# Kernel tuning notes

Hardware: AMD Instinct MI355X
Metric: run time of the kernel (lower is better)

## Reference

```python
import jax, jax.numpy as jnp
import numpy as np

N_NODES = 50000
N_EDGES = 600000
D_IN = 128
D_HID = 128
D_OUT = 128
LN_EPS = 1e-5


def _layer_norm(h, g, b):
    mu = jnp.mean(h, axis=-1, keepdims=True)
    var = jnp.var(h, axis=-1, keepdims=True)
    return (h - mu) * jax.lax.rsqrt(var + LN_EPS) * g + b


def _gin_conv(x, src, dst, w1, b1, w2, b2):
    # sum-aggregate neighbor messages at destination nodes, eps = 0
    agg = jax.ops.segment_sum(x[src], dst, num_segments=x.shape[0])
    h = x + agg
    h = jax.nn.relu(h @ w1 + b1)
    return h @ w2 + b2


def setup_inputs() -> dict:
    key = jax.random.key(0)
    ks = jax.random.split(key, 20)
    x = jax.random.normal(ks[0], (N_NODES, D_IN), dtype=jnp.float32)
    edge_index = jax.random.randint(ks[1], (2, N_EDGES), 0, N_NODES, dtype=jnp.int64)
    dims = [(D_IN, D_HID), (D_HID, D_HID), (D_HID, D_HID), (D_HID, D_OUT)]
    inp = {"x": x, "edge_index": edge_index}
    for i, (din, dout) in enumerate(dims):
        s1 = 1.0 / np.sqrt(din)
        s2 = 1.0 / np.sqrt(D_HID)
        inp[f"w1_{i}"] = jax.random.uniform(ks[2 + 4 * i], (din, D_HID), jnp.float32, -s1, s1)
        inp[f"b1_{i}"] = jax.random.uniform(ks[3 + 4 * i], (D_HID,), jnp.float32, -s1, s1)
        inp[f"w2_{i}"] = jax.random.uniform(ks[4 + 4 * i], (D_HID, dout), jnp.float32, -s2, s2)
        inp[f"b2_{i}"] = jax.random.uniform(ks[5 + 4 * i], (dout,), jnp.float32, -s2, s2)
    for i in range(3):  # LayerNorm only on first 3 blocks
        inp[f"g_{i}"] = jnp.ones((D_HID,), jnp.float32)
        inp[f"beta_{i}"] = jnp.zeros((D_HID,), jnp.float32)
    return inp


def reference(x, edge_index,
              w1_0, b1_0, w2_0, b2_0,
              w1_1, b1_1, w2_1, b2_1,
              w1_2, b1_2, w2_2, b2_2,
              w1_3, b1_3, w2_3, b2_3,
              g_0, beta_0, g_1, beta_1, g_2, beta_2):
    src, dst = edge_index[0], edge_index[1]
    mlps = [(w1_0, b1_0, w2_0, b2_0), (w1_1, b1_1, w2_1, b2_1),
            (w1_2, b1_2, w2_2, b2_2), (w1_3, b1_3, w2_3, b2_3)]
    lns = [(g_0, beta_0), (g_1, beta_1), (g_2, beta_2)]
    h = x
    for i in range(3):
        h = _gin_conv(h, src, dst, *mlps[i])
        h = _layer_norm(h, *lns[i])
        h = jax.nn.relu(h)  # dropout rate 0.0 -> identity
    h = _gin_conv(h, src, dst, *mlps[3])  # final block: no norm/act
    return h
```

## Files before the change

### kernel.cpp

```cpp
#include <hip/hip_runtime.h>
#include <hip/hip_bf16.h>

#define NN 50000
#define NE 600000
#define DD 128
#define LDSW 136
#define NB 196
#define BSH 8
#define EPB 2048
#define NBLK_AC ((NE + EPB - 1) / EPB)

typedef __bf16 bf16;
typedef __attribute__((ext_vector_type(8))) __bf16 bf16x8;
typedef __attribute__((ext_vector_type(4))) float f32x4;
typedef __attribute__((ext_vector_type(4))) unsigned int u32x4;
typedef __attribute__((ext_vector_type(4))) unsigned short u16x4;
typedef unsigned short u16;

__device__ __forceinline__ float bf_lo(unsigned int u) {
    return __builtin_bit_cast(float, u << 16);
}
__device__ __forceinline__ float bf_hi(unsigned int u) {
    return __builtin_bit_cast(float, u & 0xffff0000u);
}
__device__ __forceinline__ unsigned int bf_pack(float x, float y) {
    u16 a = __builtin_bit_cast(u16, (bf16)x);
    u16 b = __builtin_bit_cast(u16, (bf16)y);
    return (unsigned int)a | ((unsigned int)b << 16);
}

struct Ptr8 { const float* p[8]; };

__device__ __forceinline__ int edge_dst(const int* ei, int e, int f) {
    return f ? ei[2 * NE + 2 * e] : ei[NE + e];
}
__device__ __forceinline__ int edge_src(const int* ei, int e, int f) {
    return f ? ei[2 * e] : ei[e];
}

#define J1 (NN * DD / 4)
#define J2 (J1 + 8 * DD * DD)

__global__ __launch_bounds__(256) void k_init(const float* __restrict__ x,
                                              u16* __restrict__ xb,
                                              Ptr8 ws, u16* __restrict__ wt,
                                              int* __restrict__ bcnt,
                                              const int* __restrict__ ei,
                                              int* __restrict__ flag) {
    int tid = threadIdx.x;
    if (blockIdx.x == 0) {
        if (tid == 0) flag[0] = 1;
        __syncthreads();
        if (ei[2 * tid + 1] != 0) flag[0] = 0;
    }
    int id = blockIdx.x * 256 + tid;
    if (id < NB) bcnt[id] = 0;
    if (id < J1) {
        f32x4 v = *(const f32x4*)(x + (size_t)id * 4);
        u16x4 o;
        o.x = __builtin_bit_cast(u16, (bf16)v.x);
        o.y = __builtin_bit_cast(u16, (bf16)v.y);
        o.z = __builtin_bit_cast(u16, (bf16)v.z);
        o.w = __builtin_bit_cast(u16, (bf16)v.w);
        *(u16x4*)(xb + (size_t)id * 4) = o;
    } else if (id < J2) {
        int i = id - J1;
        int m = i >> 14;
        int rem = i & 16383;
        int k = rem >> 7;
        int n = rem & 127;
        bf16 b = (bf16)ws.p[m][k * DD + n];
        wt[(size_t)m * DD * DD + n * DD + k] = __builtin_bit_cast(u16, b);
    }
}

__global__ __launch_bounds__(256) void k_bcount(const int* __restrict__ ei,
                                                const int* __restrict__ flag,
                                                int* __restrict__ bcnt) {
    __shared__ int lh[NB];
    int tid = threadIdx.x;
    if (tid < NB) lh[tid] = 0;
    __syncthreads();
    int f = flag[0];
#pragma unroll
    for (int k = 0; k < 8; k++) {
        int e = blockIdx.x * EPB + k * 256 + tid;
        if (e < NE) {
            int d = edge_dst(ei, e, f);
            atomicAdd(&lh[d >> BSH], 1);
        }
    }
    __syncthreads();
    if (tid < NB && lh[tid] > 0) atomicAdd(&bcnt[tid], lh[tid]);
}

__global__ __launch_bounds__(256) void k_bscan(const int* __restrict__ bcnt,
                                               int* __restrict__ boff,
                                               int* __restrict__ bcur) {
    int tid = threadIdx.x;
    int lane = tid & 63, w = tid >> 6;
    int v = (tid < NB) ? bcnt[tid] : 0;
    int orig = v;
#pragma unroll
    for (int off = 1; off < 64; off <<= 1) {
        int t = __shfl_up(v, off);
        if (lane >= off) v += t;
    }
    __shared__ int sm[4];
    if (lane == 63) sm[w] = v;
    __syncthreads();
    int add = 0;
    for (int k = 0; k < w; k++) add += sm[k];
    int ex = v - orig + add;
    if (tid < NB) { boff[tid] = ex; bcur[tid] = ex; }
    if (tid == 0) boff[NB] = NE;
}

__global__ __launch_bounds__(256) void k_bscatter(const int* __restrict__ ei,
                                                  const int* __restrict__ flag,
                                                  int* __restrict__ bcur,
                                                  unsigned int* __restrict__ tmp) {
    __shared__ int lh[NB];
    __shared__ int gb[NB];
    int tid = threadIdx.x;
    if (tid < NB) lh[tid] = 0;
    __syncthreads();
    int f = flag[0];
    int src[8], dst[8], lp[8];
    bool val[8];
#pragma unroll
    for (int k = 0; k < 8; k++) {
        int e = blockIdx.x * EPB + k * 256 + tid;
        val[k] = (e < NE);
        if (val[k]) {
            src[k] = edge_src(ei, e, f);
            dst[k] = edge_dst(ei, e, f);
            lp[k] = atomicAdd(&lh[dst[k] >> BSH], 1);
        }
    }
    __syncthreads();
    if (tid < NB && lh[tid] > 0) gb[tid] = atomicAdd(&bcur[tid], lh[tid]);
    __syncthreads();
#pragma unroll
    for (int k = 0; k < 8; k++) {
        if (val[k]) {
            unsigned int pk = (unsigned)src[k] | ((unsigned)(dst[k] & 255) << 16);
            tmp[gb[dst[k] >> BSH] + lp[k]] = pk;
        }
    }
}

__global__ __launch_bounds__(256) void k_build(const unsigned int* __restrict__ tmp,
                                               const int* __restrict__ boff,
                                               int* __restrict__ row_start,
                                               int* __restrict__ adj) {
    __shared__ int cnt[256];
    __shared__ int ccur[256];
    __shared__ int sm[4];
    int b = blockIdx.x, tid = threadIdx.x;
    int base = b << BSH;
    int s = boff[b], e = boff[b + 1];
    cnt[tid] = 0;
    __syncthreads();
    for (int i = s + tid; i < e; i += 256) {
        atomicAdd(&cnt[tmp[i] >> 16], 1);
    }
    __syncthreads();
    int v = cnt[tid];
    int orig = v;
    int lane = tid & 63, w = tid >> 6;
#pragma unroll
    for (int off = 1; off < 64; off <<= 1) {
        int t = __shfl_up(v, off);
        if (lane >= off) v += t;
    }
    if (lane == 63) sm[w] = v;
    __syncthreads();
    int add = 0;
    for (int k = 0; k < w; k++) add += sm[k];
    int ex = s + (v - orig) + add;
    ccur[tid] = ex;
    if (base + tid < NN) row_start[base + tid] = ex;
    if (b == 0 && tid == 0) row_start[NN] = NE;
    __syncthreads();
    for (int i = s + tid; i < e; i += 256) {
        unsigned int pk = tmp[i];
        int p = atomicAdd(&ccur[pk >> 16], 1);
        adj[p] = (int)(pk & 0xffffu);
    }
}

__global__ __launch_bounds__(256) void k_agg(const u16* __restrict__ xb,
                                             const int* __restrict__ row_start,
                                             const int* __restrict__ adj,
                                             u16* __restrict__ out) {
    int gid = blockIdx.x * blockDim.x + threadIdx.x;
    int wave = gid >> 6, lane = gid & 63;
    int grp = lane >> 4, l = lane & 15;
    int node = wave * 4 + grp;
    if (node >= NN) return;
    const u32x4* base = (const u32x4*)xb;
    u32x4 sv = base[(size_t)node * 16 + l];
    float af[8], bf[8];
#pragma unroll
    for (int j = 0; j < 4; j++) {
        af[2 * j] = bf_lo(sv[j]); af[2 * j + 1] = bf_hi(sv[j]);
        bf[2 * j] = 0.f; bf[2 * j + 1] = 0.f;
    }
    int s = row_start[node], e = row_start[node + 1];
    int i = s;
    for (; i + 3 < e; i += 4) {
        u32x4 t0 = base[(size_t)adj[i] * 16 + l];
        u32x4 t1 = base[(size_t)adj[i + 1] * 16 + l];
        u32x4 t2 = base[(size_t)adj[i + 2] * 16 + l];
        u32x4 t3 = base[(size_t)adj[i + 3] * 16 + l];
#pragma unroll
        for (int j = 0; j < 4; j++) {
            af[2 * j]     += bf_lo(t0[j]) + bf_lo(t1[j]);
            af[2 * j + 1] += bf_hi(t0[j]) + bf_hi(t1[j]);
            bf[2 * j]     += bf_lo(t2[j]) + bf_lo(t3[j]);
            bf[2 * j + 1] += bf_hi(t2[j]) + bf_hi(t3[j]);
        }
    }
    for (; i < e; i++) {
        u32x4 t = base[(size_t)adj[i] * 16 + l];
#pragma unroll
        for (int j = 0; j < 4; j++) { af[2 * j] += bf_lo(t[j]); af[2 * j + 1] += bf_hi(t[j]); }
    }
    u32x4 o;
#pragma unroll
    for (int j = 0; j < 4; j++) o[j] = bf_pack(af[2 * j] + bf[2 * j], af[2 * j + 1] + bf[2 * j + 1]);
    ((u32x4*)out)[(size_t)node * 16 + l] = o;
}

template <bool LN, bool B16OUT>
__global__ __launch_bounds__(128) void k_mlp(const u16* __restrict__ hin,
                                             const u16* __restrict__ w1t,
                                             const float* __restrict__ b1,
                                             const u16* __restrict__ w2t,
                                             const float* __restrict__ b2,
                                             const float* __restrict__ g,
                                             const float* __restrict__ bta,
                                             void* __restrict__ hout) {
    __shared__ u16 lds[64 * LDSW];
    const int tid = threadIdx.x;
    const int wv = tid >> 6, lane = tid & 63;
    const int l15 = lane & 15, l4 = lane >> 4;
    const int tile0 = blockIdx.x * 64;

#pragma unroll
    for (int it = 0; it < 8; ++it) {
        int slot = tid + it * 128;
        int row = slot >> 4, c16 = slot & 15;
        u32x4 v = {0u, 0u, 0u, 0u};
        int grow = tile0 + row;
        if (grow < NN) v = *(const u32x4*)(hin + (size_t)grow * DD + c16 * 8);
        *(u32x4*)&lds[row * LDSW + c16 * 8] = v;
    }
    __syncthreads();

    float b1c[8], b2c[8], gc[8], bc[8];
#pragma unroll
    for (int c = 0; c < 8; c++) {
        int col = c * 16 + l15;
        b1c[c] = b1[col];
        b2c[c] = b2[col];
        if (LN) { gc[c] = g[col]; bc[c] = bta[col]; }
    }

    f32x4 acc[2][8];
#pragma unroll
    for (int r = 0; r < 2; r++)
#pragma unroll
        for (int c = 0; c < 8; c++) acc[r][c] = (f32x4){0.f, 0.f, 0.f, 0.f};

    const int rowbase = wv * 32;

#pragma unroll
    for (int ks = 0; ks < 4; ++ks) {
        bf16x8 a0 = __builtin_bit_cast(bf16x8,
            *(const u32x4*)&lds[(rowbase + l15) * LDSW + ks * 32 + l4 * 8]);
        bf16x8 a1 = __builtin_bit_cast(bf16x8,
            *(const u32x4*)&lds[(rowbase + 16 + l15) * LDSW + ks * 32 + l4 * 8]);
#pragma unroll
        for (int c = 0; c < 8; c++) {
            bf16x8 b = __builtin_bit_cast(bf16x8,
                *(const u32x4*)(w1t + (size_t)(c * 16 + l15) * DD + ks * 32 + l4 * 8));
            acc[0][c] = __builtin_amdgcn_mfma_f32_16x16x32_bf16(a0, b, acc[0][c], 0, 0, 0);
            acc[1][c] = __builtin_amdgcn_mfma_f32_16x16x32_bf16(a1, b, acc[1][c], 0, 0, 0);
        }
    }

#pragma unroll
    for (int r = 0; r < 2; r++) {
#pragma unroll
        for (int c = 0; c < 8; c++) {
            int col = c * 16 + l15;
#pragma unroll
            for (int j = 0; j < 4; j++) {
                float v = acc[r][c][j] + b1c[c];
                v = v > 0.f ? v : 0.f;
                bf16 b = (bf16)v;
                int row = rowbase + r * 16 + l4 * 4 + j;
                lds[row * LDSW + col] = __builtin_bit_cast(u16, b);
            }
        }
    }

#pragma unroll
    for (int r = 0; r < 2; r++)
#pragma unroll
        for (int c = 0; c < 8; c++) acc[r][c] = (f32x4){0.f, 0.f, 0.f, 0.f};

#pragma unroll
    for (int ks = 0; ks < 4; ++ks) {
        bf16x8 a0 = __builtin_bit_cast(bf16x8,
            *(const u32x4*)&lds[(rowbase + l15) * LDSW + ks * 32 + l4 * 8]);
        bf16x8 a1 = __builtin_bit_cast(bf16x8,
            *(const u32x4*)&lds[(rowbase + 16 + l15) * LDSW + ks * 32 + l4 * 8]);
#pragma unroll
        for (int c = 0; c < 8; c++) {
            bf16x8 b = __builtin_bit_cast(bf16x8,
                *(const u32x4*)(w2t + (size_t)(c * 16 + l15) * DD + ks * 32 + l4 * 8));
            acc[0][c] = __builtin_amdgcn_mfma_f32_16x16x32_bf16(a0, b, acc[0][c], 0, 0, 0);
            acc[1][c] = __builtin_amdgcn_mfma_f32_16x16x32_bf16(a1, b, acc[1][c], 0, 0, 0);
        }
    }

#pragma unroll
    for (int r = 0; r < 2; r++) {
        float vals[8][4];
#pragma unroll
        for (int c = 0; c < 8; c++)
#pragma unroll
            for (int j = 0; j < 4; j++) vals[c][j] = acc[r][c][j] + b2c[c];

        if (LN) {
            float s[4], q[4];
#pragma unroll
            for (int j = 0; j < 4; j++) {
                s[j] = 0.f; q[j] = 0.f;
#pragma unroll
                for (int c = 0; c < 8; c++) {
                    s[j] += vals[c][j];
                    q[j] += vals[c][j] * vals[c][j];
                }
            }
#pragma unroll
            for (int m = 1; m <= 8; m <<= 1) {
#pragma unroll
                for (int j = 0; j < 4; j++) {
                    s[j] += __shfl_xor(s[j], m);
                    q[j] += __shfl_xor(q[j], m);
                }
            }
#pragma unroll
            for (int j = 0; j < 4; j++) {
                float mu = s[j] * (1.f / 128.f);
                float var = q[j] * (1.f / 128.f) - mu * mu;
                float rs = rsqrtf(var + 1e-5f);
#pragma unroll
                for (int c = 0; c < 8; c++) {
                    float v = (vals[c][j] - mu) * rs * gc[c] + bc[c];
                    vals[c][j] = v > 0.f ? v : 0.f;
                }
            }
        }

#pragma unroll
        for (int c = 0; c < 8; c++) {
            int col = c * 16 + l15;
#pragma unroll
            for (int j = 0; j < 4; j++) {
                int row = tile0 + rowbase + r * 16 + l4 * 4 + j;
                if (row < NN) {
                    if (B16OUT) {
                        ((u16*)hout)[(size_t)row * DD + col] =
                            __builtin_bit_cast(u16, (bf16)vals[c][j]);
                    } else {
                        ((float*)hout)[(size_t)row * DD + col] = vals[c][j];
                    }
                }
            }
        }
    }
}

extern "C" void kernel_launch(void* const* d_in, const int* in_sizes, int n_in,
                              void* d_out, int out_size, void* d_ws, size_t ws_size,
                              hipStream_t stream) {
    const float* x = (const float*)d_in[0];
    const int* ei = (const int*)d_in[1];
    const float* w1[4]; const float* b1[4]; const float* w2[4]; const float* b2[4];
    for (int i = 0; i < 4; i++) {
        w1[i] = (const float*)d_in[2 + 4 * i];
        b1[i] = (const float*)d_in[3 + 4 * i];
        w2[i] = (const float*)d_in[4 + 4 * i];
        b2[i] = (const float*)d_in[5 + 4 * i];
    }
    const float* g[3]; const float* bt[3];
    for (int i = 0; i < 3; i++) {
        g[i] = (const float*)d_in[18 + 2 * i];
        bt[i] = (const float*)d_in[19 + 2 * i];
    }

    char* ws = (char*)d_ws;
    size_t off = 0;
    auto alloc = [&](size_t bytes) -> char* {
        char* p = ws + off;
        off = (off + bytes + 255) & ~(size_t)255;
        return p;
    };
    int* flag          = (int*)alloc(4);
    int* row_start     = (int*)alloc((NN + 1) * 4);
    int* bcnt          = (int*)alloc(NB * 4);
    int* boff          = (int*)alloc((NB + 1) * 4);
    int* bcur          = (int*)alloc(NB * 4);
    int* adj           = (int*)alloc(NE * 4);
    unsigned int* tmp  = (unsigned int*)alloc((size_t)NE * 4);
    u16* wt            = (u16*)alloc((size_t)8 * DD * DD * 2);
    u16* xb            = (u16*)alloc((size_t)NN * DD * 2);
    u16* hbf           = (u16*)alloc((size_t)NN * DD * 2);
    u16* hA            = (u16*)alloc((size_t)NN * DD * 2);
    u16* hB            = (u16*)alloc((size_t)NN * DD * 2);

    Ptr8 p8;
    for (int i = 0; i < 4; i++) {
        p8.p[2 * i] = w1[i];
        p8.p[2 * i + 1] = w2[i];
    }

    k_init<<<(J2 + 255) / 256, 256, 0, stream>>>(x, xb, p8, wt, bcnt, ei, flag);
    k_bcount<<<NBLK_AC, 256, 0, stream>>>(ei, flag, bcnt);
    k_bscan<<<1, 256, 0, stream>>>(bcnt, boff, bcur);
    k_bscatter<<<NBLK_AC, 256, 0, stream>>>(ei, flag, bcur, tmp);
    k_build<<<NB, 256, 0, stream>>>(tmp, boff, row_start, adj);

    const int mgrid = (NN + 63) / 64;
    const u16* hin = xb;
    for (int i = 0; i < 4; i++) {
        k_agg<<<(NN / 4 * 64) / 256, 256, 0, stream>>>(hin, row_start, adj, hbf);
        const u16* w1ti = wt + (size_t)(2 * i) * DD * DD;
        const u16* w2ti = wt + (size_t)(2 * i + 1) * DD * DD;
        if (i < 3) {
            u16* outp = (i & 1) ? hB : hA;
            k_mlp<true, true><<<mgrid, 128, 0, stream>>>(
                hbf, w1ti, b1[i], w2ti, b2[i], g[i], bt[i], outp);
            hin = outp;
        } else {
            k_mlp<false, false><<<mgrid, 128, 0, stream>>>(
                hbf, w1ti, b1[i], w2ti, b2[i], nullptr, nullptr, d_out);
        }
    }
}
```

Baseline: 235.1 us.

## Fold bucket scan into scatter/build, unroll aggregation by 8, stage bf16 output via LDS

Removes the single-block bucket-scan kernel by recomputing the bucket prefix sums inside the scatter and build kernels, with bcur now zeroed in init and acting as a relative offset. The neighbor aggregation loop gains an 8-way unrolled path so more gathers are in flight per iteration. The MLP kernel's bf16 output is written to LDS first and then stored to global memory as coalesced 16-byte rows instead of scattered 2-byte stores. This saves one launch and improves store efficiency, at the cost of redundant scan work in every block and extra register pressure in the aggregation loop.

```diff
diff --git a/kernel.cpp b/kernel.cpp
--- a/kernel.cpp
+++ b/kernel.cpp
@@ -45,6 +45,7 @@
                                               u16* __restrict__ xb,
                                               Ptr8 ws, u16* __restrict__ wt,
                                               int* __restrict__ bcnt,
+                                              int* __restrict__ bcur,
                                               const int* __restrict__ ei,
                                               int* __restrict__ flag) {
     int tid = threadIdx.x;
@@ -54,7 +55,7 @@
         if (ei[2 * tid + 1] != 0) flag[0] = 0;
     }
     int id = blockIdx.x * 256 + tid;
-    if (id < NB) bcnt[id] = 0;
+    if (id < NB) { bcnt[id] = 0; bcur[id] = 0; }
     if (id < J1) {
         f32x4 v = *(const f32x4*)(x + (size_t)id * 4);
         u16x4 o;
@@ -94,34 +95,15 @@
     if (tid < NB && lh[tid] > 0) atomicAdd(&bcnt[tid], lh[tid]);
 }
 
-__global__ __launch_bounds__(256) void k_bscan(const int* __restrict__ bcnt,
-                                               int* __restrict__ boff,
-                                               int* __restrict__ bcur) {
-    int tid = threadIdx.x;
-    int lane = tid & 63, w = tid >> 6;
-    int v = (tid < NB) ? bcnt[tid] : 0;
-    int orig = v;
-#pragma unroll
-    for (int off = 1; off < 64; off <<= 1) {
-        int t = __shfl_up(v, off);
-        if (lane >= off) v += t;
-    }
-    __shared__ int sm[4];
-    if (lane == 63) sm[w] = v;
-    __syncthreads();
-    int add = 0;
-    for (int k = 0; k < w; k++) add += sm[k];
-    int ex = v - orig + add;
-    if (tid < NB) { boff[tid] = ex; bcur[tid] = ex; }
-    if (tid == 0) boff[NB] = NE;
-}
-
 __global__ __launch_bounds__(256) void k_bscatter(const int* __restrict__ ei,
                                                   const int* __restrict__ flag,
+                                                  const int* __restrict__ bcnt,
                                                   int* __restrict__ bcur,
                                                   unsigned int* __restrict__ tmp) {
     __shared__ int lh[NB];
     __shared__ int gb[NB];
+    __shared__ int sboff[NB];
+    __shared__ int sm[4];
     int tid = threadIdx.x;
     if (tid < NB) lh[tid] = 0;
     __syncthreads();
@@ -139,7 +121,24 @@
         }
     }
     __syncthreads();
-    if (tid < NB && lh[tid] > 0) gb[tid] = atomicAdd(&bcur[tid], lh[tid]);
+    {
+        int lane = tid & 63, w = tid >> 6;
+        int v = (tid < NB) ? bcnt[tid] : 0;
+        int orig = v;
+#pragma unroll
+        for (int off = 1; off < 64; off <<= 1) {
+            int t = __shfl_up(v, off);
+            if (lane >= off) v += t;
+        }
+        if (lane == 63) sm[w] = v;
+        __syncthreads();
+        int add = 0;
+        for (int k = 0; k < w; k++) add += sm[k];
+        if (tid < NB) sboff[tid] = v - orig + add;
+    }
+    __syncthreads();
+    if (tid < NB && lh[tid] > 0)
+        gb[tid] = sboff[tid] + atomicAdd(&bcur[tid], lh[tid]);
     __syncthreads();
 #pragma unroll
     for (int k = 0; k < 8; k++) {
@@ -151,7 +150,7 @@
 }
 
 __global__ __launch_bounds__(256) void k_build(const unsigned int* __restrict__ tmp,
-                                               const int* __restrict__ boff,
+                                               const int* __restrict__ bcnt,
                                                int* __restrict__ row_start,
                                                int* __restrict__ adj) {
     __shared__ int cnt[256];
@@ -159,26 +158,31 @@
     __shared__ int sm[4];
     int b = blockIdx.x, tid = threadIdx.x;
     int base = b << BSH;
-    int s = boff[b], e = boff[b + 1];
+    int lane = tid & 63, w = tid >> 6;
     cnt[tid] = 0;
-    __syncthreads();
+    int v = (tid < b) ? bcnt[tid] : 0;
+#pragma unroll
+    for (int off = 1; off < 64; off <<= 1) v += __shfl_xor(v, off);
+    if (lane == 0) sm[w] = v;
+    __syncthreads();
+    int s = sm[0] + sm[1] + sm[2] + sm[3];
+    int e = s + bcnt[b];
     for (int i = s + tid; i < e; i += 256) {
         atomicAdd(&cnt[tmp[i] >> 16], 1);
     }
     __syncthreads();
-    int v = cnt[tid];
-    int orig = v;
-    int lane = tid & 63, w = tid >> 6;
+    int v2 = cnt[tid];
+    int orig = v2;
 #pragma unroll
     for (int off = 1; off < 64; off <<= 1) {
-        int t = __shfl_up(v, off);
-        if (lane >= off) v += t;
-    }
-    if (lane == 63) sm[w] = v;
+        int t = __shfl_up(v2, off);
+        if (lane >= off) v2 += t;
+    }
+    if (lane == 63) sm[w] = v2;
     __syncthreads();
     int add = 0;
     for (int k = 0; k < w; k++) add += sm[k];
-    int ex = s + (v - orig) + add;
+    int ex = s + (v2 - orig) + add;
     ccur[tid] = ex;
     if (base + tid < NN) row_start[base + tid] = ex;
     if (b == 0 && tid == 0) row_start[NN] = NE;
@@ -209,6 +213,23 @@
     }
     int s = row_start[node], e = row_start[node + 1];
     int i = s;
+    for (; i + 7 < e; i += 8) {
+        u32x4 t0 = base[(size_t)adj[i] * 16 + l];
+        u32x4 t1 = base[(size_t)adj[i + 1] * 16 + l];
+        u32x4 t2 = base[(size_t)adj[i + 2] * 16 + l];
+        u32x4 t3 = base[(size_t)adj[i + 3] * 16 + l];
+        u32x4 t4 = base[(size_t)adj[i + 4] * 16 + l];
+        u32x4 t5 = base[(size_t)adj[i + 5] * 16 + l];
+        u32x4 t6 = base[(size_t)adj[i + 6] * 16 + l];
+        u32x4 t7 = base[(size_t)adj[i + 7] * 16 + l];
+#pragma unroll
+        for (int j = 0; j < 4; j++) {
+            af[2 * j]     += (bf_lo(t0[j]) + bf_lo(t1[j])) + (bf_lo(t2[j]) + bf_lo(t3[j]));
+            af[2 * j + 1] += (bf_hi(t0[j]) + bf_hi(t1[j])) + (bf_hi(t2[j]) + bf_hi(t3[j]));
+            bf[2 * j]     += (bf_lo(t4[j]) + bf_lo(t5[j])) + (bf_lo(t6[j]) + bf_lo(t7[j]));
+            bf[2 * j + 1] += (bf_hi(t4[j]) + bf_hi(t5[j])) + (bf_hi(t6[j]) + bf_hi(t7[j]));
+        }
+    }
     for (; i + 3 < e; i += 4) {
         u32x4 t0 = base[(size_t)adj[i] * 16 + l];
         u32x4 t1 = base[(size_t)adj[i + 1] * 16 + l];
@@ -367,21 +388,41 @@
             }
         }
 
-#pragma unroll
-        for (int c = 0; c < 8; c++) {
-            int col = c * 16 + l15;
-#pragma unroll
-            for (int j = 0; j < 4; j++) {
-                int row = tile0 + rowbase + r * 16 + l4 * 4 + j;
-                if (row < NN) {
-                    if (B16OUT) {
-                        ((u16*)hout)[(size_t)row * DD + col] =
-                            __builtin_bit_cast(u16, (bf16)vals[c][j]);
-                    } else {
+        if (B16OUT) {
+#pragma unroll
+            for (int c = 0; c < 8; c++) {
+                int col = c * 16 + l15;
+#pragma unroll
+                for (int j = 0; j < 4; j++) {
+                    int row = rowbase + r * 16 + l4 * 4 + j;
+                    lds[row * LDSW + col] =
+                        __builtin_bit_cast(u16, (bf16)vals[c][j]);
+                }
+            }
+        } else {
+#pragma unroll
+            for (int c = 0; c < 8; c++) {
+                int col = c * 16 + l15;
+#pragma unroll
+                for (int j = 0; j < 4; j++) {
+                    int row = tile0 + rowbase + r * 16 + l4 * 4 + j;
+                    if (row < NN)
                         ((float*)hout)[(size_t)row * DD + col] = vals[c][j];
-                    }
                 }
             }
+        }
+    }
+
+    if (B16OUT) {
+#pragma unroll
+        for (int it = 0; it < 8; ++it) {
+            int slot = it * 64 + lane;
+            int row = rowbase + (slot >> 4);
+            int c16 = slot & 15;
+            u32x4 v = *(const u32x4*)&lds[row * LDSW + c16 * 8];
+            int grow = tile0 + row;
+            if (grow < NN)
+                *(u32x4*)((u16*)hout + (size_t)grow * DD + c16 * 8) = v;
         }
     }
 }
@@ -414,7 +455,6 @@
     int* flag          = (int*)alloc(4);
     int* row_start     = (int*)alloc((NN + 1) * 4);
     int* bcnt          = (int*)alloc(NB * 4);
-    int* boff          = (int*)alloc((NB + 1) * 4);
     int* bcur          = (int*)alloc(NB * 4);
     int* adj           = (int*)alloc(NE * 4);
     unsigned int* tmp  = (unsigned int*)alloc((size_t)NE * 4);
@@ -430,11 +470,10 @@
         p8.p[2 * i + 1] = w2[i];
     }
 
-    k_init<<<(J2 + 255) / 256, 256, 0, stream>>>(x, xb, p8, wt, bcnt, ei, flag);
+    k_init<<<(J2 + 255) / 256, 256, 0, stream>>>(x, xb, p8, wt, bcnt, bcur, ei, flag);
     k_bcount<<<NBLK_AC, 256, 0, stream>>>(ei, flag, bcnt);
-    k_bscan<<<1, 256, 0, stream>>>(bcnt, boff, bcur);
-    k_bscatter<<<NBLK_AC, 256, 0, stream>>>(ei, flag, bcur, tmp);
-    k_build<<<NB, 256, 0, stream>>>(tmp, boff, row_start, adj);
+    k_bscatter<<<NBLK_AC, 256, 0, stream>>>(ei, flag, bcnt, bcur, tmp);
+    k_build<<<NB, 256, 0, stream>>>(tmp, bcnt, row_start, adj);
 
     const int mgrid = (NN + 63) / 64;
     const u16* hin = xb;
```

Result: no change. 238.1 us (+1.3%).
